# Kernel tuning notes

Measured on AMD Instinct MI355X. Metric: run time of the kernel, lower is better.

## Reference

```python
import jax, jax.numpy as jnp
import numpy as np

B, S, D = 16, 2048, 1024   # batch, src_len, per-tensor feature dim (input_dim*growth_factor)
OUT = 1024                 # output_dim


def setup_inputs() -> dict:
    key = jax.random.key(0)
    k1, k2, k3, k4, k5, k6 = jax.random.split(key, 6)
    hidden = jax.random.normal(k1, (B, S, D), dtype=jnp.float32)
    encoder_outputs = jax.random.normal(k2, (B, S, D), dtype=jnp.float32)
    c_t = jax.random.normal(k3, (B, D), dtype=jnp.float32)
    # Linear(input_dim*3*growth_factor=3*D, OUT): PyTorch stores weight as [OUT, 3D]
    limit = 1.0 / np.sqrt(3 * D)
    W = jax.random.uniform(k4, (OUT, 3 * D), minval=-limit, maxval=limit, dtype=jnp.float32)
    b = jax.random.uniform(k5, (OUT,), minval=-limit, maxval=limit, dtype=jnp.float32)
    v = jax.random.uniform(k6, (OUT,), dtype=jnp.float32)  # torch.rand -> U[0,1)
    return {"hidden": hidden, "encoder_outputs": encoder_outputs, "c_t": c_t,
            "W": W, "b": b, "v": v}


def reference(hidden, encoder_outputs, c_t, W, b, v):
    # c_t broadcast over src_len; concat on feature dim -> [B, S, 3D]
    c_rep = jnp.broadcast_to(c_t[:, None, :], hidden.shape)
    cat = jnp.concatenate((hidden, c_rep, encoder_outputs), axis=2)
    # energy = relu(cat @ W^T + b): [B, S, OUT]
    energy = jax.nn.relu(jnp.einsum('bsf,of->bso', cat, W) + b)
    # attention = energy @ v: [B, S], then softmax over src_len
    attention = jnp.einsum('bso,o->bs', energy, v)
    return jax.nn.softmax(attention, axis=1)
```

## Files before the change

### kernel.cpp

```cpp
#include <hip/hip_runtime.h>
#include <hip/hip_bf16.h>


typedef __attribute__((ext_vector_type(8))) short short8;
typedef __attribute__((ext_vector_type(4))) float f32x4;
typedef __attribute__((ext_vector_type(8))) unsigned short ushort8v;
typedef __attribute__((ext_vector_type(4))) unsigned short ushort4v;

#define NB 16
#define NS 2048
#define ND 1024
#define NOUT 1024
#define NM (NB * NS)
#define KHE 2048
#define TM 256
#define TN 128
#define BK 64
#define NROWS (TM + TN)

#define PREP_ACONV 16384
#define PREP_WCONV 2048
#define PREP_CBIAS 256
#define PREP_ZERO 32

__device__ __forceinline__ unsigned short bf16_rne(float x) {
    unsigned int u = __float_as_uint(x);
    unsigned int r = (u + 0x7fffu + ((u >> 16) & 1u)) >> 16;
    return (unsigned short)r;
}

__device__ __forceinline__ void gload_lds16(const unsigned short* g, unsigned short* l) {
    __builtin_amdgcn_global_load_lds(
        (const __attribute__((address_space(1))) void*)g,
        (__attribute__((address_space(3))) void*)l, 16, 0, 0);
}

__global__ __launch_bounds__(256) void prep_k(const float* __restrict__ hidden,
                                              const float* __restrict__ enc,
                                              const float* __restrict__ c_t,
                                              const float* __restrict__ W,
                                              const float* __restrict__ bias,
                                              unsigned short* __restrict__ Abf,
                                              unsigned short* __restrict__ Wbf,
                                              float* __restrict__ cbias,
                                              float* __restrict__ logits) {
    const int bid = blockIdx.x;
    const int tid = threadIdx.x;
    if (bid < PREP_ACONV) {
        size_t c = (size_t)bid * 256 + tid;
        size_t m = c >> 7;
        int k = (int)(c & 127) * 16;
        const float* src = (k < ND) ? (hidden + m * ND + k) : (enc + m * ND + (k - ND));
        float4 f0 = ((const float4*)src)[0];
        float4 f1 = ((const float4*)src)[1];
        float4 f2 = ((const float4*)src)[2];
        float4 f3 = ((const float4*)src)[3];
        ushort8v h0, h1;
        h0[0] = bf16_rne(f0.x); h0[1] = bf16_rne(f0.y); h0[2] = bf16_rne(f0.z); h0[3] = bf16_rne(f0.w);
        h0[4] = bf16_rne(f1.x); h0[5] = bf16_rne(f1.y); h0[6] = bf16_rne(f1.z); h0[7] = bf16_rne(f1.w);
        h1[0] = bf16_rne(f2.x); h1[1] = bf16_rne(f2.y); h1[2] = bf16_rne(f2.z); h1[3] = bf16_rne(f2.w);
        h1[4] = bf16_rne(f3.x); h1[5] = bf16_rne(f3.y); h1[6] = bf16_rne(f3.z); h1[7] = bf16_rne(f3.w);
        *(ushort8v*)(Abf + m * KHE + k) = h0;
        *(ushort8v*)(Abf + m * KHE + k + 8) = h1;
    } else if (bid < PREP_ACONV + PREP_WCONV) {
        int idx = (bid - PREP_ACONV) * 256 + tid;
        int o = idx >> 9;
        int k = (idx & 511) * 4;
        int off = (k < ND) ? k : (k + ND);
        float4 f = *(const float4*)(W + (size_t)o * 3072 + off);
        ushort4v h;
        h.x = bf16_rne(f.x); h.y = bf16_rne(f.y); h.z = bf16_rne(f.z); h.w = bf16_rne(f.w);
        *(ushort4v*)(Wbf + (size_t)o * KHE + k) = h;
    } else if (bid < PREP_ACONV + PREP_WCONV + PREP_CBIAS) {
        int o = (bid - PREP_ACONV - PREP_WCONV) * 4 + (tid >> 6);
        int lane = tid & 63;
        const float* w = W + (size_t)o * 3072 + ND;
        float wr[16];
        #pragma unroll
        for (int j = 0; j < 16; ++j) wr[j] = w[lane + j * 64];
        float bo = bias[o];
        for (int b = 0; b < NB; ++b) {
            const float* cc = c_t + (size_t)b * ND;
            float s = 0.f;
            #pragma unroll
            for (int j = 0; j < 16; ++j) s = fmaf(cc[lane + j * 64], wr[j], s);
            #pragma unroll
            for (int m = 1; m < 64; m <<= 1) s += __shfl_xor(s, m);
            if (lane == 0) cbias[b * NOUT + o] = s + bo;
        }
    } else {
        int idx = (bid - PREP_ACONV - PREP_WCONV - PREP_CBIAS) * 256 + tid;
        ((float4*)logits)[idx] = make_float4(0.f, 0.f, 0.f, 0.f);
    }
}

__global__ __launch_bounds__(256) void wconv_k(const float* __restrict__ W,
                                               unsigned short* __restrict__ Wbf) {
    int idx = blockIdx.x * 256 + threadIdx.x;
    int o = idx >> 9;
    int k = (idx & 511) * 4;
    int off = (k < ND) ? k : (k + ND);
    float4 f = *(const float4*)(W + (size_t)o * 3072 + off);
    ushort4v h;
    h.x = bf16_rne(f.x); h.y = bf16_rne(f.y); h.z = bf16_rne(f.z); h.w = bf16_rne(f.w);
    *(ushort4v*)(Wbf + (size_t)o * KHE + k) = h;
}

__global__ __launch_bounds__(256) void cbias_k(const float* __restrict__ c_t,
                                               const float* __restrict__ W,
                                               const float* __restrict__ bias,
                                               float* __restrict__ cbias) {
    int o = blockIdx.x * 4 + (threadIdx.x >> 6);
    int lane = threadIdx.x & 63;
    const float* w = W + (size_t)o * 3072 + ND;
    float wr[16];
    #pragma unroll
    for (int j = 0; j < 16; ++j) wr[j] = w[lane + j * 64];
    float bo = bias[o];
    for (int b = 0; b < NB; ++b) {
        const float* c = c_t + (size_t)b * ND;
        float s = 0.f;
        #pragma unroll
        for (int j = 0; j < 16; ++j) s = fmaf(c[lane + j * 64], wr[j], s);
        #pragma unroll
        for (int m = 1; m < 64; m <<= 1) s += __shfl_xor(s, m);
        if (lane == 0) cbias[b * NOUT + o] = s + bo;
    }
}

__global__ __launch_bounds__(512, 4) void gemm_att_bf_k(const unsigned short* __restrict__ Abf,
                                                        const unsigned short* __restrict__ Wbf,
                                                        const float* __restrict__ cbias,
                                                        const float* __restrict__ v,
                                                        float* __restrict__ logits) {
    __shared__ unsigned short Ls[NROWS * BK] __attribute__((aligned(16)));
    __shared__ float rowsum[2][TM];
    __shared__ float cb_s[TN];
    __shared__ float v_s[TN];

    const int tid = threadIdx.x;
    const int bid = blockIdx.x;
    const int ntile = bid & 7;
    const int mtile = bid >> 3;
    const int m0 = mtile * TM;
    const int o0 = ntile * TN;
    const int batch = m0 >> 11;

    if (tid < TN) {
        cb_s[tid] = cbias[batch * NOUT + o0 + tid];
        v_s[tid] = v[o0 + tid];
    }

    const int wid = tid >> 6;
    const int lane = tid & 63;
    const int wm = (wid & 3) * 64;
    const int wn = (wid >> 2) * 64;

    const int srow = lane >> 3;
    const int schunk = (lane & 7) ^ srow;

    f32x4 acc[4][4] = {};

    for (int kt = 0; kt < KHE; kt += BK) {
        #pragma unroll
        for (int t = 0; t < 6; ++t) {
            const int r0 = wid * 48 + t * 8;
            const unsigned short* src = (r0 < TM)
                ? (Abf + (size_t)(m0 + r0 + srow) * KHE + kt + schunk * 8)
                : (Wbf + (size_t)(o0 + r0 - TM + srow) * KHE + kt + schunk * 8);
            gload_lds16(src, Ls + r0 * BK);
        }
        __syncthreads();

        #pragma unroll
        for (int s = 0; s < 2; ++s) {
            const int cbase = s * 4 + (lane >> 4);
            short8 a_frag[4], b_frag[4];
            #pragma unroll
            for (int i = 0; i < 4; ++i) {
                int row = wm + i * 16 + (lane & 15);
                a_frag[i] = *(const short8*)(Ls + row * BK + ((cbase ^ (row & 7)) * 8));
            }
            #pragma unroll
            for (int j = 0; j < 4; ++j) {
                int row = TM + wn + j * 16 + (lane & 15);
                b_frag[j] = *(const short8*)(Ls + row * BK + ((cbase ^ (row & 7)) * 8));
            }
            #pragma unroll
            for (int i = 0; i < 4; ++i)
                #pragma unroll
                for (int j = 0; j < 4; ++j)
                    acc[i][j] = __builtin_amdgcn_mfma_f32_16x16x32_bf16(a_frag[i], b_frag[j],
                                                                        acc[i][j], 0, 0, 0);
        }
        __syncthreads();
    }

    const int col = lane & 15;
    const int q = lane >> 4;
    float vv[4], cbv[4];
    #pragma unroll
    for (int j = 0; j < 4; ++j) {
        int oc = wn + j * 16 + col;
        vv[j] = v_s[oc];
        cbv[j] = cb_s[oc];
    }
    #pragma unroll
    for (int i = 0; i < 4; ++i) {
        #pragma unroll
        for (int r = 0; r < 4; ++r) {
            float s = 0.f;
            #pragma unroll
            for (int j = 0; j < 4; ++j) {
                float e = acc[i][j][r] + cbv[j];
                e = fmaxf(e, 0.f);
                s = fmaf(e, vv[j], s);
            }
            s += __shfl_xor(s, 1);
            s += __shfl_xor(s, 2);
            s += __shfl_xor(s, 4);
            s += __shfl_xor(s, 8);
            if (col == 0) rowsum[wid >> 2][wm + i * 16 + q * 4 + r] = s;
        }
    }
    __syncthreads();
    if (tid < TM) atomicAdd(&logits[m0 + tid], rowsum[0][tid] + rowsum[1][tid]);
}

__global__ __launch_bounds__(256) void gemm_att_k(const float* __restrict__ hidden,
                                                  const float* __restrict__ enc,
                                                  const unsigned short* __restrict__ Wbf,
                                                  const float* __restrict__ Wf,
                                                  const float* __restrict__ cbias,
                                                  const float* __restrict__ v,
                                                  float* __restrict__ logits,
                                                  int use_wbf) {
    __shared__ unsigned short As[128 * 32] __attribute__((aligned(16)));
    __shared__ unsigned short Bs[128 * 32] __attribute__((aligned(16)));
    __shared__ float rowsum[2][128];
    __shared__ float cb_s[128];
    __shared__ float v_s[128];

    const int tid = threadIdx.x;
    const int ntile = blockIdx.x & 7;
    const int mtile = blockIdx.x >> 3;
    const int m0 = mtile * 128;
    const int o0 = ntile * 128;
    const int batch = m0 >> 11;

    if (tid < 128) {
        cb_s[tid] = cbias[batch * NOUT + o0 + tid];
        v_s[tid] = v[o0 + tid];
    }

    const int wid = tid >> 6;
    const int lane = tid & 63;
    const int wm = (wid & 1) * 64;
    const int wn = (wid >> 1) * 64;

    f32x4 acc[4][4] = {};

    for (int kt = 0; kt < KHE; kt += 32) {
        const float* Abase = (kt < ND) ? hidden : enc;
        const int aoff = (kt < ND) ? kt : (kt - ND);
        #pragma unroll
        for (int i = 0; i < 4; ++i) {
            int p = tid + i * 256;
            int row = p >> 3, kc = p & 7;
            float4 f = *(const float4*)(Abase + (size_t)(m0 + row) * ND + aoff + kc * 4);
            ushort4v h;
            h.x = bf16_rne(f.x); h.y = bf16_rne(f.y); h.z = bf16_rne(f.z); h.w = bf16_rne(f.w);
            *(ushort4v*)(As + row * 32 + kc * 4) = h;
        }
        if (use_wbf) {
            #pragma unroll
            for (int i = 0; i < 2; ++i) {
                int u = tid + i * 256;
                int ol = u >> 2, kc = u & 3;
                ushort8v w8 = *(const ushort8v*)(Wbf + (size_t)(o0 + ol) * KHE + kt + kc * 8);
                *(ushort8v*)(Bs + ol * 32 + kc * 8) = w8;
            }
        } else {
            const int woff = (kt < ND) ? kt : (kt + ND);
            #pragma unroll
            for (int i = 0; i < 4; ++i) {
                int p = tid + i * 256;
                int row = p >> 3, kc = p & 7;
                float4 f = *(const float4*)(Wf + (size_t)(o0 + row) * 3072 + woff + kc * 4);
                ushort4v h;
                h.x = bf16_rne(f.x); h.y = bf16_rne(f.y); h.z = bf16_rne(f.z); h.w = bf16_rne(f.w);
                *(ushort4v*)(Bs + row * 32 + kc * 4) = h;
            }
        }
        __syncthreads();

        short8 a_frag[4], b_frag[4];
        #pragma unroll
        for (int i = 0; i < 4; ++i)
            a_frag[i] = *(const short8*)(As + (wm + i * 16 + (lane & 15)) * 32 + (lane >> 4) * 8);
        #pragma unroll
        for (int j = 0; j < 4; ++j)
            b_frag[j] = *(const short8*)(Bs + (wn + j * 16 + (lane & 15)) * 32 + (lane >> 4) * 8);
        #pragma unroll
        for (int i = 0; i < 4; ++i)
            #pragma unroll
            for (int j = 0; j < 4; ++j)
                acc[i][j] = __builtin_amdgcn_mfma_f32_16x16x32_bf16(a_frag[i], b_frag[j],
                                                                    acc[i][j], 0, 0, 0);
        __syncthreads();
    }

    const int col = lane & 15;
    const int q = lane >> 4;
    float vv[4], cbv[4];
    #pragma unroll
    for (int j = 0; j < 4; ++j) {
        int oc = wn + j * 16 + col;
        vv[j] = v_s[oc];
        cbv[j] = cb_s[oc];
    }
    #pragma unroll
    for (int i = 0; i < 4; ++i) {
        #pragma unroll
        for (int r = 0; r < 4; ++r) {
            float s = 0.f;
            #pragma unroll
            for (int j = 0; j < 4; ++j) {
                float e = acc[i][j][r] + cbv[j];
                e = fmaxf(e, 0.f);
                s = fmaf(e, vv[j], s);
            }
            s += __shfl_xor(s, 1);
            s += __shfl_xor(s, 2);
            s += __shfl_xor(s, 4);
            s += __shfl_xor(s, 8);
            if (col == 0) rowsum[wid >> 1][wm + i * 16 + q * 4 + r] = s;
        }
    }
    __syncthreads();
    if (tid < 128) atomicAdd(&logits[m0 + tid], rowsum[0][tid] + rowsum[1][tid]);
}

__global__ __launch_bounds__(256) void softmax_k(const float* __restrict__ logits,
                                                 float* __restrict__ out) {
    const int b = blockIdx.x;
    const int tid = threadIdx.x;
    const int lane = tid & 63, wid = tid >> 6;
    __shared__ float redmax[4];
    __shared__ float redsum[4];
    const float* L = logits + (size_t)b * NS;
    float x[8];
    float mx = -3.4e38f;
    #pragma unroll
    for (int i = 0; i < 8; ++i) {
        x[i] = L[tid + i * 256];
        mx = fmaxf(mx, x[i]);
    }
    #pragma unroll
    for (int m = 1; m < 64; m <<= 1) mx = fmaxf(mx, __shfl_xor(mx, m));
    if (lane == 0) redmax[wid] = mx;
    __syncthreads();
    mx = fmaxf(fmaxf(redmax[0], redmax[1]), fmaxf(redmax[2], redmax[3]));
    float sum = 0.f;
    #pragma unroll
    for (int i = 0; i < 8; ++i) {
        x[i] = expf(x[i] - mx);
        sum += x[i];
    }
    #pragma unroll
    for (int m = 1; m < 64; m <<= 1) sum += __shfl_xor(sum, m);
    if (lane == 0) redsum[wid] = sum;
    __syncthreads();
    float inv = 1.0f / (redsum[0] + redsum[1] + redsum[2] + redsum[3]);
    #pragma unroll
    for (int i = 0; i < 8; ++i) out[(size_t)b * NS + tid + i * 256] = x[i] * inv;
}

extern "C" void kernel_launch(void* const* d_in, const int* in_sizes, int n_in,
                              void* d_out, int out_size, void* d_ws, size_t ws_size,
                              hipStream_t stream) {
    const float* hidden = (const float*)d_in[0];
    const float* enc    = (const float*)d_in[1];
    const float* c_t    = (const float*)d_in[2];
    const float* W      = (const float*)d_in[3];
    const float* bias   = (const float*)d_in[4];
    const float* v      = (const float*)d_in[5];
    float* out = (float*)d_out;

    char* ws = (char*)d_ws;
    float* logits = (float*)ws;
    float* cbias  = (float*)(ws + 131072);
    unsigned short* Wbf = (unsigned short*)(ws + 196608);
    unsigned short* Abf = (unsigned short*)(ws + 196608 + 4194304);
    const size_t need_wbf = 196608 + (size_t)NOUT * KHE * 2;
    const size_t need_abf = need_wbf + (size_t)NM * KHE * 2;

    if (ws_size >= need_abf) {
        prep_k<<<PREP_ACONV + PREP_WCONV + PREP_CBIAS + PREP_ZERO, 256, 0, stream>>>(
            hidden, enc, c_t, W, bias, Abf, Wbf, cbias, logits);
        gemm_att_bf_k<<<(NM / TM) * (NOUT / TN), 512, 0, stream>>>(Abf, Wbf, cbias, v, logits);
    } else if (ws_size >= need_wbf) {
        hipMemsetAsync(logits, 0, NM * sizeof(float), stream);
        cbias_k<<<NOUT / 4, 256, 0, stream>>>(c_t, W, bias, cbias);
        wconv_k<<<(NOUT * KHE / 4) / 256, 256, 0, stream>>>(W, Wbf);
        gemm_att_k<<<(NM / 128) * (NOUT / 128), 256, 0, stream>>>(hidden, enc, Wbf, W, cbias, v,
                                                                  logits, 1);
    } else {
        hipMemsetAsync(logits, 0, NM * sizeof(float), stream);
        cbias_k<<<NOUT / 4, 256, 0, stream>>>(c_t, W, bias, cbias);
        gemm_att_k<<<(NM / 128) * (NOUT / 128), 256, 0, stream>>>(hidden, enc, Wbf, W, cbias, v,
                                                                  logits, 0);
    }
    softmax_k<<<NB, 256, 0, stream>>>(logits, out);
}
```

Measured before the change: 457.4 us.

## Replace bf16 GEMM with 256x256 double-buffered, phase-interleaved 8-wave kernel

Replaces the single-buffered 256x128 tile GEMM with a 256x256 tile kernel that double-buffers LDS. Each k-step is split into four phases, and each phase issues the global->LDS prefetch for the next tile while running one quadrant of MFMAs, using explicit vmcnt waits and barriers. MFMA sections also get raised wave priority. The aim is to hide global-load latency behind compute and raise arithmetic intensity per tile. The cost is roughly double the LDS footprint and more accumulator registers, which lowers occupancy to 2 blocks per CU, and the hand-counted waitcnt values could be fragile.

```diff
diff --git a/kernel.cpp b/kernel.cpp
--- a/kernel.cpp
+++ b/kernel.cpp
@@ -13,10 +13,11 @@
 #define NOUT 1024
 #define NM (NB * NS)
 #define KHE 2048
-#define TM 256
-#define TN 128
-#define BK 64
-#define NROWS (TM + TN)
+
+#define B8M 256
+#define B8N 256
+#define B8K 64
+#define NT8 (KHE / B8K)
 
 #define PREP_ACONV 16384
 #define PREP_WCONV 2048
@@ -33,6 +34,12 @@
     __builtin_amdgcn_global_load_lds(
         (const __attribute__((address_space(1))) void*)g,
         (__attribute__((address_space(3))) void*)l, 16, 0, 0);
+}
+
+__device__ __forceinline__ void bar_fence() {
+    asm volatile("" ::: "memory");
+    __builtin_amdgcn_s_barrier();
+    asm volatile("" ::: "memory");
 }
 
 __global__ __launch_bounds__(256) void prep_k(const float* __restrict__ hidden,
@@ -128,85 +135,143 @@
     }
 }
 
-__global__ __launch_bounds__(512, 4) void gemm_att_bf_k(const unsigned short* __restrict__ Abf,
-                                                        const unsigned short* __restrict__ Wbf,
-                                                        const float* __restrict__ cbias,
-                                                        const float* __restrict__ v,
-                                                        float* __restrict__ logits) {
-    __shared__ unsigned short Ls[NROWS * BK] __attribute__((aligned(16)));
-    __shared__ float rowsum[2][TM];
-    __shared__ float cb_s[TN];
-    __shared__ float v_s[TN];
+__global__ __launch_bounds__(512, 2) void gemm8_k(const unsigned short* __restrict__ Abf,
+                                                  const unsigned short* __restrict__ Wbf,
+                                                  const float* __restrict__ cbias,
+                                                  const float* __restrict__ v,
+                                                  float* __restrict__ logits) {
+    __shared__ unsigned short Ls[2][512][B8K] __attribute__((aligned(16)));
+    __shared__ float rowsum[4][B8M];
+    __shared__ float cb_s[B8N];
+    __shared__ float v_s[B8N];
 
     const int tid = threadIdx.x;
-    const int bid = blockIdx.x;
-    const int ntile = bid & 7;
-    const int mtile = bid >> 3;
-    const int m0 = mtile * TM;
-    const int o0 = ntile * TN;
+    const int ntile = blockIdx.x & 3;
+    const int mtile = blockIdx.x >> 2;
+    const int m0 = mtile * B8M;
+    const int o0 = ntile * B8N;
     const int batch = m0 >> 11;
 
-    if (tid < TN) {
+    if (tid < B8N) {
         cb_s[tid] = cbias[batch * NOUT + o0 + tid];
         v_s[tid] = v[o0 + tid];
     }
 
     const int wid = tid >> 6;
     const int lane = tid & 63;
-    const int wm = (wid & 3) * 64;
-    const int wn = (wid >> 2) * 64;
-
-    const int srow = lane >> 3;
-    const int schunk = (lane & 7) ^ srow;
-
-    f32x4 acc[4][4] = {};
-
-    for (int kt = 0; kt < KHE; kt += BK) {
-        #pragma unroll
-        for (int t = 0; t < 6; ++t) {
-            const int r0 = wid * 48 + t * 8;
-            const unsigned short* src = (r0 < TM)
-                ? (Abf + (size_t)(m0 + r0 + srow) * KHE + kt + schunk * 8)
-                : (Wbf + (size_t)(o0 + r0 - TM + srow) * KHE + kt + schunk * 8);
-            gload_lds16(src, Ls + r0 * BK);
-        }
-        __syncthreads();
-
-        #pragma unroll
-        for (int s = 0; s < 2; ++s) {
-            const int cbase = s * 4 + (lane >> 4);
-            short8 a_frag[4], b_frag[4];
+    const int wm = (wid & 1) * 128;
+    const int wn = (wid >> 1) * 64;
+    const int lr = lane >> 3;
+    const int lc = (lane & 7) ^ lr;
+
+    f32x4 acc[8][4] = {};
+    short8 a[4][2], b[2][2];
+
+    auto stageA = [&](int buf, int kt, int h) {
+        #pragma unroll
+        for (int t = 0; t < 2; ++t) {
+            const int r0 = t * 128 + h * 64 + wid * 8;
+            gload_lds16(Abf + (size_t)(m0 + r0 + lr) * KHE + kt + lc * 8, &Ls[buf][r0][0]);
+        }
+    };
+    auto stageB = [&](int buf, int kt, int h) {
+        #pragma unroll
+        for (int t = 0; t < 2; ++t) {
+            const int r0 = (wid >> 1) * 64 + h * 32 + (wid & 1) * 8 + t * 16;
+            gload_lds16(Wbf + (size_t)(o0 + r0 + lr) * KHE + kt + lc * 8, &Ls[buf][256 + r0][0]);
+        }
+    };
+    auto loadA = [&](int buf, int mh) {
+        #pragma unroll
+        for (int ks = 0; ks < 2; ++ks) {
+            const int cb = ks * 4 + (lane >> 4);
             #pragma unroll
             for (int i = 0; i < 4; ++i) {
-                int row = wm + i * 16 + (lane & 15);
-                a_frag[i] = *(const short8*)(Ls + row * BK + ((cbase ^ (row & 7)) * 8));
-            }
-            #pragma unroll
-            for (int j = 0; j < 4; ++j) {
-                int row = TM + wn + j * 16 + (lane & 15);
-                b_frag[j] = *(const short8*)(Ls + row * BK + ((cbase ^ (row & 7)) * 8));
-            }
+                const int row = wm + mh * 64 + i * 16 + (lane & 15);
+                a[i][ks] = *(const short8*)&Ls[buf][row][(cb ^ (row & 7)) * 8];
+            }
+        }
+    };
+    auto loadB = [&](int buf, int nh) {
+        #pragma unroll
+        for (int ks = 0; ks < 2; ++ks) {
+            const int cb = ks * 4 + (lane >> 4);
+            #pragma unroll
+            for (int j = 0; j < 2; ++j) {
+                const int row = wn + nh * 32 + j * 16 + (lane & 15);
+                b[j][ks] = *(const short8*)&Ls[buf][256 + row][(cb ^ (row & 7)) * 8];
+            }
+        }
+    };
+    auto mfma16 = [&](int mh, int nh) {
+        __builtin_amdgcn_s_setprio(1);
+        #pragma unroll
+        for (int ks = 0; ks < 2; ++ks)
             #pragma unroll
             for (int i = 0; i < 4; ++i)
                 #pragma unroll
-                for (int j = 0; j < 4; ++j)
-                    acc[i][j] = __builtin_amdgcn_mfma_f32_16x16x32_bf16(a_frag[i], b_frag[j],
-                                                                        acc[i][j], 0, 0, 0);
-        }
-        __syncthreads();
-    }
+                for (int j = 0; j < 2; ++j)
+                    acc[mh * 4 + i][nh * 2 + j] = __builtin_amdgcn_mfma_f32_16x16x32_bf16(
+                        a[i][ks], b[j][ks], acc[mh * 4 + i][nh * 2 + j], 0, 0, 0);
+        __builtin_amdgcn_s_setprio(0);
+    };
+
+    stageA(0, 0, 0);
+    stageB(0, 0, 0);
+    stageB(0, 0, 1);
+    stageA(0, 0, 1);
+    asm volatile("s_waitcnt vmcnt(2)" ::: "memory");
+    __builtin_amdgcn_s_barrier();
+    asm volatile("" ::: "memory");
+
+    #pragma unroll 2
+    for (int t = 0; t < NT8; ++t) {
+        const int cur = t & 1, nxt = cur ^ 1;
+        const int kt1 = (t + 1) * B8K;
+        const bool pf = (t + 1 < NT8);
+
+        loadA(cur, 0);
+        loadB(cur, 0);
+        if (pf) stageA(nxt, kt1, 0);
+        bar_fence();
+        mfma16(0, 0);
+        bar_fence();
+
+        loadB(cur, 1);
+        if (pf) stageB(nxt, kt1, 0);
+        bar_fence();
+        mfma16(0, 1);
+        if (pf) asm volatile("s_waitcnt vmcnt(4)" ::: "memory");
+        else    asm volatile("s_waitcnt vmcnt(0)" ::: "memory");
+        bar_fence();
+
+        loadA(cur, 1);
+        if (pf) stageB(nxt, kt1, 1);
+        bar_fence();
+        mfma16(1, 1);
+        bar_fence();
+
+        loadB(cur, 0);
+        if (pf) stageA(nxt, kt1, 1);
+        bar_fence();
+        mfma16(1, 0);
+        asm volatile("s_waitcnt vmcnt(2)" ::: "memory");
+        bar_fence();
+    }
+
+    __syncthreads();
 
     const int col = lane & 15;
     const int q = lane >> 4;
     float vv[4], cbv[4];
     #pragma unroll
     for (int j = 0; j < 4; ++j) {
-        int oc = wn + j * 16 + col;
+        const int oc = wn + j * 16 + col;
         vv[j] = v_s[oc];
         cbv[j] = cb_s[oc];
     }
     #pragma unroll
-    for (int i = 0; i < 4; ++i) {
+    for (int i = 0; i < 8; ++i) {
         #pragma unroll
         for (int r = 0; r < 4; ++r) {
             float s = 0.f;
@@ -220,11 +285,13 @@
             s += __shfl_xor(s, 2);
             s += __shfl_xor(s, 4);
             s += __shfl_xor(s, 8);
-            if (col == 0) rowsum[wid >> 2][wm + i * 16 + q * 4 + r] = s;
+            if (col == 0) rowsum[wid >> 1][wm + i * 16 + q * 4 + r] = s;
         }
     }
     __syncthreads();
-    if (tid < TM) atomicAdd(&logits[m0 + tid], rowsum[0][tid] + rowsum[1][tid]);
+    if (tid < B8M)
+        atomicAdd(&logits[m0 + tid],
+                  rowsum[0][tid] + rowsum[1][tid] + rowsum[2][tid] + rowsum[3][tid]);
 }
 
 __global__ __launch_bounds__(256) void gemm_att_k(const float* __restrict__ hidden,
@@ -398,7 +465,7 @@
     if (ws_size >= need_abf) {
         prep_k<<<PREP_ACONV + PREP_WCONV + PREP_CBIAS + PREP_ZERO, 256, 0, stream>>>(
             hidden, enc, c_t, W, bias, Abf, Wbf, cbias, logits);
-        gemm_att_bf_k<<<(NM / TM) * (NOUT / TN), 512, 0, stream>>>(Abf, Wbf, cbias, v, logits);
+        gemm8_k<<<(NM / B8M) * (NOUT / B8N), 512, 0, stream>>>(Abf, Wbf, cbias, v, logits);
     } else if (ws_size >= need_wbf) {
         hipMemsetAsync(logits, 0, NM * sizeof(float), stream);
         cbias_k<<<NOUT / 4, 256, 0, stream>>>(c_t, W, bias, cbias);
```

Result: faster. 443.4 us (-3.1%).
